# Kernel tuning notes

Measured on AMD Instinct MI355X. Metric: run time of the kernel, lower is better.

Reference implementation:

```python
import jax, jax.numpy as jnp
import numpy as np

B, N, D_MODEL, H, D_K, D_V = 4, 1024, 1024, 16, 64, 1024  # N == D_V required by the module's output matmul


def setup_inputs() -> dict:
    key = jax.random.key(0)
    ks = jax.random.split(key, 7)
    def xavier(k, shape):
        fan_in, fan_out = shape[-2], shape[-1]
        std = (2.0 / (fan_in + fan_out)) ** 0.5
        return jax.random.normal(k, shape, dtype=jnp.float32) * std
    return {
        "query": jax.random.normal(ks[0], (B, N, D_MODEL), dtype=jnp.float32),
        "key": jax.random.normal(ks[1], (B, N, D_MODEL), dtype=jnp.float32),
        "value": jax.random.normal(ks[2], (B, N, D_MODEL), dtype=jnp.float32),
        "w_q": xavier(ks[3], (H, D_MODEL, D_K)),
        "w_k": xavier(ks[4], (H, D_MODEL, D_K)),
        "w_v": xavier(ks[5], (H, D_MODEL, D_V)),
        "w_o": xavier(ks[6], (D_MODEL, H * D_V)),
    }


def reference(query, key, value, w_q, w_k, w_v, w_o):
    # Per-head projections: [B,N,d_model] x [H,d_model,d] -> [B,H,N,d]
    q = jnp.einsum('bnd,hdk->bhnk', query, w_q)
    k = jnp.einsum('bnd,hdk->bhnk', key, w_k)
    v = jnp.einsum('bnd,hdv->bhnv', value, w_v)
    scale = 1.0 / jnp.sqrt(jnp.asarray(q.shape[-1], q.dtype))
    scores = jnp.einsum('bhqk,bhmk->bhqm', q, k) * scale  # [B,H,N,N]
    weights = jax.nn.softmax(scores, axis=-1)
    out = jnp.einsum('bhqm,bhmv->bhqv', weights, v)  # [B,H,N,d_v]
    out = out.reshape(out.shape[0], -1, out.shape[-1])  # [B, H*N, d_v]
    # Faithful to source: torch.matmul(w_o, output) with w_o [d_model, H*d_v];
    # requires H*d_v == H*N (N == d_v); result [B, d_model, d_v].
    return jnp.einsum('de,bev->bdv', w_o, out)
```

## Files before the change

### kernel.cpp

```cpp
#include <hip/hip_runtime.h>
#include <hip/hip_bf16.h>

typedef __hip_bfloat16 bf16;
typedef __attribute__((ext_vector_type(8))) short short8;
typedef __attribute__((ext_vector_type(4))) float floatx4;

#define BK 64
#define LDK 72

__device__ __forceinline__ void gload_lds16(const void* g, void* l) {
    __builtin_amdgcn_global_load_lds(
        (const __attribute__((address_space(1))) void*)g,
        (__attribute__((address_space(3))) void*)l, 16, 0, 0);
}

template<bool OUT_BF16>
__global__ void __launch_bounds__(512) gemm_nt_256(
    const bf16* __restrict__ A, const bf16* __restrict__ B, void* __restrict__ Cv,
    int K, int lda, int ldb, int ldc,
    long sA, long sB, long sC)
{
    __shared__ __align__(16) bf16 As[2][256 * 64];
    __shared__ __align__(16) bf16 Bs[2][256 * 64];

    int bx = blockIdx.x, by = blockIdx.y, bz = blockIdx.z;
    if (gridDim.x == 4 && gridDim.y == 4 && (gridDim.z & 7) == 0) {
        int hw  = bx + (by << 2) + (bz << 4);
        int xcd = hw & 7;
        int idx = hw >> 3;
        int per = (int)(gridDim.z >> 3) << 4;
        int nh  = xcd * per + idx;
        bx = nh & 3; by = (nh >> 2) & 3; bz = nh >> 4;
    }

    long aoff = (long)bz * sA + (long)by * 256 * lda;
    long boff = (long)bz * sB + (long)bx * 256 * ldb;
    long coff = (long)bz * sC;

    int tid  = threadIdx.x;
    int lane = tid & 63;
    int wave = tid >> 6;
    int quad = lane >> 4;
    int l16  = lane & 15;
    int swz  = l16 & 7;
    int wm = (wave >> 2) * 128;
    int wn = (wave & 3) * 64;

    int srow   = tid >> 3;
    int schunk = (tid & 7) ^ (srow & 7);
    int dwb    = (wave << 3) * 64;

    const bf16* Asrc = A + aoff;
    const bf16* Bsrc = B + boff;

    floatx4 acc[8][4] = {};
    const int nt = K / BK;

    auto STAGE_A = [&](int db, int half, int kt) {
        long kofs = (long)kt * BK + schunk * 8;
#pragma unroll
        for (int s = 0; s < 2; s++) {
            int r = half * 128 + s * 64;
            gload_lds16(Asrc + (long)(r + srow) * lda + kofs, &As[db][r * 64 + dwb]);
        }
    };
    auto STAGE_B = [&](int db, int half, int kt) {
        long kofs = (long)kt * BK + schunk * 8;
#pragma unroll
        for (int s = 0; s < 2; s++) {
            int r = half * 128 + s * 64;
            gload_lds16(Bsrc + (long)(r + srow) * ldb + kofs, &Bs[db][r * 64 + dwb]);
        }
    };

    STAGE_A(0, 0, 0); STAGE_A(0, 1, 0); STAGE_B(0, 0, 0); STAGE_B(0, 1, 0);
    STAGE_A(1, 0, 1);
    asm volatile("s_waitcnt vmcnt(2)" ::: "memory");
    asm volatile("s_barrier" ::: "memory");

    short8 af[4][2], bf[4][2];
    int db = 0;
    for (int kt = 0; kt < nt; kt++) {
        const bf16* as = As[db];
        const bf16* bs = Bs[db];
        bool st1 = (kt + 1 < nt);
        bool st2 = (kt + 2 < nt);

#pragma unroll
        for (int i = 0; i < 4; i++)
#pragma unroll
            for (int ks = 0; ks < 2; ks++)
                af[i][ks] = *(const short8*)(&as[(wm + i * 16 + l16) * 64 + ((((ks << 2) | quad)) ^ swz) * 8]);
#pragma unroll
        for (int j = 0; j < 2; j++)
#pragma unroll
            for (int ks = 0; ks < 2; ks++)
                bf[j][ks] = *(const short8*)(&bs[(wn + j * 16 + l16) * 64 + ((((ks << 2) | quad)) ^ swz) * 8]);
        if (st1) STAGE_A(db ^ 1, 1, kt + 1);
        __builtin_amdgcn_sched_barrier(0);
        __builtin_amdgcn_s_setprio(1);
#pragma unroll
        for (int i = 0; i < 4; i++)
#pragma unroll
            for (int j = 0; j < 2; j++)
#pragma unroll
                for (int ks = 0; ks < 2; ks++)
                    acc[i][j] = __builtin_amdgcn_mfma_f32_16x16x32_bf16(af[i][ks], bf[j][ks], acc[i][j], 0, 0, 0);
        __builtin_amdgcn_s_setprio(0);
        __builtin_amdgcn_sched_barrier(0);

#pragma unroll
        for (int j = 2; j < 4; j++)
#pragma unroll
            for (int ks = 0; ks < 2; ks++)
                bf[j][ks] = *(const short8*)(&bs[(wn + j * 16 + l16) * 64 + ((((ks << 2) | quad)) ^ swz) * 8]);
        if (st1) STAGE_B(db ^ 1, 0, kt + 1);
        __builtin_amdgcn_sched_barrier(0);
        __builtin_amdgcn_s_setprio(1);
#pragma unroll
        for (int i = 0; i < 4; i++)
#pragma unroll
            for (int j = 2; j < 4; j++)
#pragma unroll
                for (int ks = 0; ks < 2; ks++)
                    acc[i][j] = __builtin_amdgcn_mfma_f32_16x16x32_bf16(af[i][ks], bf[j][ks], acc[i][j], 0, 0, 0);
        __builtin_amdgcn_s_setprio(0);
        __builtin_amdgcn_sched_barrier(0);

#pragma unroll
        for (int i = 0; i < 4; i++)
#pragma unroll
            for (int ks = 0; ks < 2; ks++)
                af[i][ks] = *(const short8*)(&as[(wm + 64 + i * 16 + l16) * 64 + ((((ks << 2) | quad)) ^ swz) * 8]);
        if (st1) STAGE_B(db ^ 1, 1, kt + 1);
        __builtin_amdgcn_sched_barrier(0);
        __builtin_amdgcn_s_setprio(1);
#pragma unroll
        for (int i = 0; i < 4; i++)
#pragma unroll
            for (int j = 2; j < 4; j++)
#pragma unroll
                for (int ks = 0; ks < 2; ks++)
                    acc[i + 4][j] = __builtin_amdgcn_mfma_f32_16x16x32_bf16(af[i][ks], bf[j][ks], acc[i + 4][j], 0, 0, 0);
        __builtin_amdgcn_s_setprio(0);
        __builtin_amdgcn_sched_barrier(0);
        asm volatile("s_barrier" ::: "memory");

        if (st2) STAGE_A(db, 0, kt + 2);
        __builtin_amdgcn_sched_barrier(0);
        __builtin_amdgcn_s_setprio(1);
#pragma unroll
        for (int i = 0; i < 4; i++)
#pragma unroll
            for (int j = 0; j < 2; j++)
#pragma unroll
                for (int ks = 0; ks < 2; ks++)
                    acc[i + 4][j] = __builtin_amdgcn_mfma_f32_16x16x32_bf16(af[i][ks], bf[j][ks], acc[i + 4][j], 0, 0, 0);
        __builtin_amdgcn_s_setprio(0);
        __builtin_amdgcn_sched_barrier(0);

        if (st2) asm volatile("s_waitcnt vmcnt(2)" ::: "memory");
        else     asm volatile("s_waitcnt vmcnt(0)" ::: "memory");
        asm volatile("s_barrier" ::: "memory");
        db ^= 1;
    }

#pragma unroll
    for (int i = 0; i < 8; i++) {
        int row = by * 256 + wm + i * 16 + quad * 4;
#pragma unroll
        for (int j = 0; j < 4; j++) {
            int col = bx * 256 + wn + j * 16 + l16;
#pragma unroll
            for (int v = 0; v < 4; v++) {
                float val = acc[i][j][v];
                if (OUT_BF16)
                    ((bf16*)Cv)[coff + (long)(row + v) * ldc + col] = __float2bfloat16(val);
                else
                    ((float*)Cv)[coff + (long)(row + v) * ldc + col] = val;
            }
        }
    }
}

template<bool OUT_BF16, bool A_F32, bool B_F32>
__global__ void __launch_bounds__(256) gemm_nt(
    const void* __restrict__ Av, const void* __restrict__ Bv, void* __restrict__ Cv,
    int M, int N, int K, int lda, int ldb, int ldc,
    long sA, long sB, long sC)
{
    __shared__ __align__(16) bf16 As[128 * LDK];
    __shared__ __align__(16) bf16 Bs[128 * LDK];

    int bx = blockIdx.x, by = blockIdx.y, bz = blockIdx.z;

    long aoff = (long)bz * sA;
    long boff = (long)bz * sB;
    long coff = (long)bz * sC;

    int m0 = by * 128;
    int n0 = bx * 128;
    int tid  = threadIdx.x;
    int lane = tid & 63;
    int wave = tid >> 6;
    int quad = lane >> 4;
    int l16  = lane & 15;
    int wm = (wave >> 1) * 64;
    int wn = (wave & 1) * 64;

    int sr = tid >> 3;
    int sc = (tid & 7) * 8;

    floatx4 acc[4][4] = {};

    uint4  pa[4], pb[4];
    float4 pa0[4], pa1[4], pb0[4], pb1[4];

    const int nt = K / BK;

#pragma unroll
    for (int s = 0; s < 4; s++) {
        int r = sr + 32 * s;
        int gm = m0 + r;
        if (A_F32) {
            const float* p = (const float*)Av + aoff + (long)gm * lda + sc;
            if (gm < M) { pa0[s] = *(const float4*)p; pa1[s] = *(const float4*)(p + 4); }
            else { pa0[s] = {0,0,0,0}; pa1[s] = {0,0,0,0}; }
        } else {
            pa[s] = (gm < M) ? *(const uint4*)((const bf16*)Av + aoff + (long)gm * lda + sc)
                             : (uint4){0,0,0,0};
        }
        int gn = n0 + r;
        if (B_F32) {
            const float* p = (const float*)Bv + boff + (long)gn * ldb + sc;
            if (gn < N) { pb0[s] = *(const float4*)p; pb1[s] = *(const float4*)(p + 4); }
            else { pb0[s] = {0,0,0,0}; pb1[s] = {0,0,0,0}; }
        } else {
            pb[s] = (gn < N) ? *(const uint4*)((const bf16*)Bv + boff + (long)gn * ldb + sc)
                             : (uint4){0,0,0,0};
        }
    }

    for (int kt = 0; kt < nt; kt++) {
        __syncthreads();
#pragma unroll
        for (int s = 0; s < 4; s++) {
            int r = sr + 32 * s;
            if (A_F32) {
                bf16 t[8];
                t[0]=__float2bfloat16(pa0[s].x); t[1]=__float2bfloat16(pa0[s].y);
                t[2]=__float2bfloat16(pa0[s].z); t[3]=__float2bfloat16(pa0[s].w);
                t[4]=__float2bfloat16(pa1[s].x); t[5]=__float2bfloat16(pa1[s].y);
                t[6]=__float2bfloat16(pa1[s].z); t[7]=__float2bfloat16(pa1[s].w);
                *(uint4*)(&As[r * LDK + sc]) = *(const uint4*)t;
            } else {
                *(uint4*)(&As[r * LDK + sc]) = pa[s];
            }
            if (B_F32) {
                bf16 t[8];
                t[0]=__float2bfloat16(pb0[s].x); t[1]=__float2bfloat16(pb0[s].y);
                t[2]=__float2bfloat16(pb0[s].z); t[3]=__float2bfloat16(pb0[s].w);
                t[4]=__float2bfloat16(pb1[s].x); t[5]=__float2bfloat16(pb1[s].y);
                t[6]=__float2bfloat16(pb1[s].z); t[7]=__float2bfloat16(pb1[s].w);
                *(uint4*)(&Bs[r * LDK + sc]) = *(const uint4*)t;
            } else {
                *(uint4*)(&Bs[r * LDK + sc]) = pb[s];
            }
        }
        __syncthreads();

        if (kt + 1 < nt) {
            int k0 = (kt + 1) * BK;
#pragma unroll
            for (int s = 0; s < 4; s++) {
                int r = sr + 32 * s;
                int gm = m0 + r;
                if (A_F32) {
                    const float* p = (const float*)Av + aoff + (long)gm * lda + k0 + sc;
                    if (gm < M) { pa0[s] = *(const float4*)p; pa1[s] = *(const float4*)(p + 4); }
                    else { pa0[s] = {0,0,0,0}; pa1[s] = {0,0,0,0}; }
                } else {
                    pa[s] = (gm < M) ? *(const uint4*)((const bf16*)Av + aoff + (long)gm * lda + k0 + sc)
                                     : (uint4){0,0,0,0};
                }
                int gn = n0 + r;
                if (B_F32) {
                    const float* p = (const float*)Bv + boff + (long)gn * ldb + k0 + sc;
                    if (gn < N) { pb0[s] = *(const float4*)p; pb1[s] = *(const float4*)(p + 4); }
                    else { pb0[s] = {0,0,0,0}; pb1[s] = {0,0,0,0}; }
                } else {
                    pb[s] = (gn < N) ? *(const uint4*)((const bf16*)Bv + boff + (long)gn * ldb + k0 + sc)
                                     : (uint4){0,0,0,0};
                }
            }
        }

#pragma unroll
        for (int ks = 0; ks < 2; ks++) {
            short8 af[4], bfr[4];
#pragma unroll
            for (int i = 0; i < 4; i++)
                af[i] = *(const short8*)(&As[(wm + i * 16 + l16) * LDK + ks * 32 + quad * 8]);
#pragma unroll
            for (int j = 0; j < 4; j++)
                bfr[j] = *(const short8*)(&Bs[(wn + j * 16 + l16) * LDK + ks * 32 + quad * 8]);
#pragma unroll
            for (int i = 0; i < 4; i++)
#pragma unroll
                for (int j = 0; j < 4; j++)
                    acc[i][j] = __builtin_amdgcn_mfma_f32_16x16x32_bf16(af[i], bfr[j], acc[i][j], 0, 0, 0);
        }
    }

#pragma unroll
    for (int i = 0; i < 4; i++) {
        int row = m0 + wm + i * 16 + quad * 4;
#pragma unroll
        for (int j = 0; j < 4; j++) {
            int col = n0 + wn + j * 16 + l16;
            if (col >= N) continue;
#pragma unroll
            for (int v = 0; v < 4; v++) {
                int r = row + v;
                if (r < M) {
                    float val = acc[i][j][v];
                    if (OUT_BF16)
                        ((bf16*)Cv)[coff + (long)r * ldc + col] = __float2bfloat16(val);
                    else
                        ((float*)Cv)[coff + (long)r * ldc + col] = val;
                }
            }
        }
    }
}

__global__ void __launch_bounds__(256) attn_softmax(
    const bf16* __restrict__ Q, const bf16* __restrict__ Kb, bf16* __restrict__ Wts)
{
    __shared__ __align__(16) bf16 Ks[64 * 72];

    int h = blockIdx.y;
    const bf16* Qbh = Q  + (long)h * 262144;
    const bf16* Kbh = Kb + (long)h * 262144;
    bf16* W = Wts + (long)h * 1048576;

    int tid  = threadIdx.x;
    int lane = tid & 63;
    int wave = tid >> 6;
    int quad = lane >> 4;
    int l16  = lane & 15;
    int q0 = blockIdx.x * 64 + wave * 16;

    short8 a0 = *(const short8*)(Qbh + (long)(q0 + l16) * 64 + quad * 8);
    short8 a1 = *(const short8*)(Qbh + (long)(q0 + l16) * 64 + 32 + quad * 8);

    int sr = tid >> 3;
    int sc = (tid & 7) * 8;

    const float scale = 0.125f;
    float m_v[4] = {-1e30f, -1e30f, -1e30f, -1e30f};
    float l_v[4] = {0.f, 0.f, 0.f, 0.f};

    for (int t = 0; t < 16; t++) {
        __syncthreads();
        const bf16* src = Kbh + (long)(t * 64 + sr) * 64 + sc;
        *(uint4*)(&Ks[sr * 72 + sc])        = *(const uint4*)src;
        *(uint4*)(&Ks[(sr + 32) * 72 + sc]) = *(const uint4*)(src + 32 * 64);
        __syncthreads();
#pragma unroll
        for (int j = 0; j < 4; j++) {
            short8 b0 = *(const short8*)(&Ks[(j * 16 + l16) * 72 + quad * 8]);
            short8 b1 = *(const short8*)(&Ks[(j * 16 + l16) * 72 + 32 + quad * 8]);
            floatx4 acc = {0.f, 0.f, 0.f, 0.f};
            acc = __builtin_amdgcn_mfma_f32_16x16x32_bf16(a0, b0, acc, 0, 0, 0);
            acc = __builtin_amdgcn_mfma_f32_16x16x32_bf16(a1, b1, acc, 0, 0, 0);
#pragma unroll
            for (int v = 0; v < 4; v++) {
                float s  = acc[v] * scale;
                float nm = fmaxf(m_v[v], s);
                l_v[v] = l_v[v] * __expf(m_v[v] - nm) + __expf(s - nm);
                m_v[v] = nm;
            }
        }
    }

#pragma unroll
    for (int d = 1; d < 16; d <<= 1) {
#pragma unroll
        for (int v = 0; v < 4; v++) {
            float om = __shfl_xor(m_v[v], d);
            float ol = __shfl_xor(l_v[v], d);
            float nm = fmaxf(m_v[v], om);
            l_v[v] = l_v[v] * __expf(m_v[v] - nm) + ol * __expf(om - nm);
            m_v[v] = nm;
        }
    }
    float linv[4];
#pragma unroll
    for (int v = 0; v < 4; v++) linv[v] = 1.0f / l_v[v];

    for (int t = 0; t < 16; t++) {
        __syncthreads();
        const bf16* src = Kbh + (long)(t * 64 + sr) * 64 + sc;
        *(uint4*)(&Ks[sr * 72 + sc])        = *(const uint4*)src;
        *(uint4*)(&Ks[(sr + 32) * 72 + sc]) = *(const uint4*)(src + 32 * 64);
        __syncthreads();
#pragma unroll
        for (int j = 0; j < 4; j++) {
            short8 b0 = *(const short8*)(&Ks[(j * 16 + l16) * 72 + quad * 8]);
            short8 b1 = *(const short8*)(&Ks[(j * 16 + l16) * 72 + 32 + quad * 8]);
            floatx4 acc = {0.f, 0.f, 0.f, 0.f};
            acc = __builtin_amdgcn_mfma_f32_16x16x32_bf16(a0, b0, acc, 0, 0, 0);
            acc = __builtin_amdgcn_mfma_f32_16x16x32_bf16(a1, b1, acc, 0, 0, 0);
#pragma unroll
            for (int v = 0; v < 4; v++) {
                float w = __expf(acc[v] * scale - m_v[v]) * linv[v];
                W[(long)(q0 + quad * 4 + v) * 1024 + t * 64 + j * 16 + l16] = __float2bfloat16(w);
            }
        }
    }
}

__global__ void __launch_bounds__(256) cast_bf16_k(
    const float* __restrict__ in, bf16* __restrict__ out, int n4)
{
    int i = blockIdx.x * 256 + threadIdx.x;
    if (i >= n4) return;
    float4 v = ((const float4*)in)[i];
    bf16 t[4] = {__float2bfloat16(v.x), __float2bfloat16(v.y),
                 __float2bfloat16(v.z), __float2bfloat16(v.w)};
    ((uint2*)out)[i] = *(const uint2*)t;
}

__global__ void __launch_bounds__(256) transpose_cast(
    const float* __restrict__ in, bf16* __restrict__ out, int R, int C)
{
    __shared__ float t[32][33];
    int h = blockIdx.z;
    const float* inh = in + (long)h * R * C;
    bf16* outh = out + (long)h * R * C;
    int c0 = blockIdx.x * 32, r0 = blockIdx.y * 32;
    int tx = threadIdx.x, ty = threadIdx.y;
#pragma unroll
    for (int i = 0; i < 32; i += 8)
        t[ty + i][tx] = inh[(long)(r0 + ty + i) * C + c0 + tx];
    __syncthreads();
#pragma unroll
    for (int i = 0; i < 32; i += 8)
        outh[(long)(c0 + ty + i) * R + r0 + tx] = __float2bfloat16(t[tx][ty + i]);
}

__global__ void __launch_bounds__(256) reduce16_k(
    const float* __restrict__ part, float* __restrict__ out)
{
    int i = blockIdx.x * 256 + threadIdx.x;
    float4 s = ((const float4*)part)[i];
#pragma unroll
    for (int c = 1; c < 16; c++) {
        float4 p = ((const float4*)part)[c * 262144 + i];
        s.x += p.x; s.y += p.y; s.z += p.z; s.w += p.w;
    }
    ((float4*)out)[i] = s;
}

extern "C" void kernel_launch(void* const* d_in, const int* in_sizes, int n_in,
                              void* d_out, int out_size, void* d_ws, size_t ws_size,
                              hipStream_t stream) {
    const float* query = (const float*)d_in[0];
    const float* key   = (const float*)d_in[1];
    const float* value = (const float*)d_in[2];
    const float* w_q   = (const float*)d_in[3];
    const float* w_k   = (const float*)d_in[4];
    const float* w_v   = (const float*)d_in[5];
    const float* w_o   = (const float*)d_in[6];
    float* out = (float*)d_out;

    char* ws = (char*)d_ws;
    const size_t MB = (size_t)1 << 20;
    bf16* wqt      = (bf16*)(ws + 0 * MB);
    bf16* wkt      = (bf16*)(ws + 2 * MB);
    bf16* wvt      = (bf16*)(ws + 4 * MB);
    bf16* wob      = (bf16*)(ws + 36 * MB);
    bf16* qb       = (bf16*)(ws + 68 * MB);
    bf16* kb       = (bf16*)(ws + 76 * MB);
    bf16* vt_b     = (bf16*)(ws + 84 * MB);
    bf16* wts_b    = (bf16*)(ws + 116 * MB);
    bf16* att_b    = (bf16*)(ws + 148 * MB);
    bf16* value_bf = (bf16*)(ws + 148 * MB);
    float* out_part = (float*)(ws + 84 * MB);

    transpose_cast<<<dim3(2, 32, 16),  dim3(32, 8), 0, stream>>>(w_q, wqt, 1024, 64);
    transpose_cast<<<dim3(2, 32, 16),  dim3(32, 8), 0, stream>>>(w_k, wkt, 1024, 64);
    transpose_cast<<<dim3(32, 32, 16), dim3(32, 8), 0, stream>>>(w_v, wvt, 1024, 1024);
    cast_bf16_k<<<16384, 256, 0, stream>>>(w_o, wob, 1024 * 16384 / 4);

    gemm_nt<true, true, false><<<dim3(1, 32, 16), 256, 0, stream>>>(
        query, wqt, qb, 4096, 64, 1024, 1024, 1024, 64, 0L, 65536L, 262144L);
    gemm_nt<true, true, false><<<dim3(1, 32, 16), 256, 0, stream>>>(
        key, wkt, kb, 4096, 64, 1024, 1024, 1024, 64, 0L, 65536L, 262144L);

    for (int b = 0; b < 4; b++) {
        cast_bf16_k<<<1024, 256, 0, stream>>>(value + (long)b * 1048576, value_bf, 262144);

        gemm_nt_256<true><<<dim3(4, 4, 16), 512, 0, stream>>>(
            wvt, value_bf, vt_b,
            1024, 1024, 1024, 1024, 1048576L, 0L, 1048576L);

        attn_softmax<<<dim3(16, 16), 256, 0, stream>>>(
            qb + (long)b * 65536, kb + (long)b * 65536, wts_b);

        gemm_nt_256<true><<<dim3(4, 4, 16), 512, 0, stream>>>(
            vt_b, wts_b, att_b,
            1024, 1024, 1024, 16384, 1048576L, 1048576L, 1024L);

        gemm_nt_256<false><<<dim3(4, 4, 16), 512, 0, stream>>>(
            wob, att_b, out_part,
            1024, 16384, 16384, 1024, 1024L, 1024L, 1048576L);

        reduce16_k<<<1024, 256, 0, stream>>>(out_part, out + (long)b * 1048576);
    }

    (void)in_sizes; (void)n_in; (void)out_size; (void)ws_size;
}
```

Measured before the change: 859.8 us.

## Deepen GEMM prefetch to two full tiles ahead with region-ordered staging

Reorganizes the global-to-LDS staging in the 256x256 bf16 GEMM so both buffers are filled up front and tile kt+2 is loaded into the current buffer as soon as each quarter of it has been consumed. Row groups of A and B are split into interleaved regions (AX/BX, then BY/AY) that match the order in which the MFMA phases read them, with waits on vmcnt(8) and barriers placed after those phases. The goal is to keep more global loads in flight and hide memory latency better. The cost is extra barriers and lgkmcnt waits inside the loop, plus tighter correctness requirements on which LDS regions are overwritten when.

```diff
diff --git a/kernel.cpp b/kernel.cpp
--- a/kernel.cpp
+++ b/kernel.cpp
@@ -48,34 +48,32 @@
 
     int srow   = tid >> 3;
     int schunk = (tid & 7) ^ (srow & 7);
-    int dwb    = (wave << 3) * 64;
 
     const bf16* Asrc = A + aoff;
     const bf16* Bsrc = B + boff;
 
+    auto STA = [&](int db, int r0, int kt) {
+        long kofs = (long)kt * BK + schunk * 8;
+        gload_lds16(Asrc + (long)(r0 + srow) * lda + kofs,
+                    &As[db][(r0 + (wave << 3)) * 64]);
+    };
+    auto STB = [&](int db, int r0, int r1, int kt) {
+        long kofs = (long)kt * BK + schunk * 8;
+        int rr = (srow < 32) ? (r0 + srow) : (r1 + srow - 32);
+        int rb = (wave < 4) ? (r0 + (wave << 3)) : (r1 + ((wave - 4) << 3));
+        gload_lds16(Bsrc + (long)rr * ldb + kofs, &Bs[db][rb * 64]);
+    };
+    auto STAGE_AX = [&](int db, int kt){ STA(db, 0, kt);  STA(db, 128, kt); };
+    auto STAGE_AY = [&](int db, int kt){ STA(db, 64, kt); STA(db, 192, kt); };
+    auto STAGE_BX = [&](int db, int kt){ STB(db, 0, 64, kt);  STB(db, 128, 192, kt); };
+    auto STAGE_BY = [&](int db, int kt){ STB(db, 32, 96, kt); STB(db, 160, 224, kt); };
+
     floatx4 acc[8][4] = {};
     const int nt = K / BK;
 
-    auto STAGE_A = [&](int db, int half, int kt) {
-        long kofs = (long)kt * BK + schunk * 8;
-#pragma unroll
-        for (int s = 0; s < 2; s++) {
-            int r = half * 128 + s * 64;
-            gload_lds16(Asrc + (long)(r + srow) * lda + kofs, &As[db][r * 64 + dwb]);
-        }
-    };
-    auto STAGE_B = [&](int db, int half, int kt) {
-        long kofs = (long)kt * BK + schunk * 8;
-#pragma unroll
-        for (int s = 0; s < 2; s++) {
-            int r = half * 128 + s * 64;
-            gload_lds16(Bsrc + (long)(r + srow) * ldb + kofs, &Bs[db][r * 64 + dwb]);
-        }
-    };
-
-    STAGE_A(0, 0, 0); STAGE_A(0, 1, 0); STAGE_B(0, 0, 0); STAGE_B(0, 1, 0);
-    STAGE_A(1, 0, 1);
-    asm volatile("s_waitcnt vmcnt(2)" ::: "memory");
+    STAGE_AX(0, 0); STAGE_BX(0, 0); STAGE_BY(0, 0); STAGE_AY(0, 0);
+    STAGE_AX(1, 1); STAGE_BX(1, 1); STAGE_BY(1, 1); STAGE_AY(1, 1);
+    asm volatile("s_waitcnt vmcnt(8)" ::: "memory");
     asm volatile("s_barrier" ::: "memory");
 
     short8 af[4][2], bf[4][2];
@@ -83,56 +81,52 @@
     for (int kt = 0; kt < nt; kt++) {
         const bf16* as = As[db];
         const bf16* bs = Bs[db];
-        bool st1 = (kt + 1 < nt);
         bool st2 = (kt + 2 < nt);
 
 #pragma unroll
         for (int i = 0; i < 4; i++)
 #pragma unroll
             for (int ks = 0; ks < 2; ks++)
-                af[i][ks] = *(const short8*)(&as[(wm + i * 16 + l16) * 64 + ((((ks << 2) | quad)) ^ swz) * 8]);
+                af[i][ks] = *(const short8*)(&as[(wm + i * 16 + l16) * 64 + (((ks << 2) | quad) ^ swz) * 8]);
 #pragma unroll
         for (int j = 0; j < 2; j++)
 #pragma unroll
             for (int ks = 0; ks < 2; ks++)
-                bf[j][ks] = *(const short8*)(&bs[(wn + j * 16 + l16) * 64 + ((((ks << 2) | quad)) ^ swz) * 8]);
-        if (st1) STAGE_A(db ^ 1, 1, kt + 1);
-        __builtin_amdgcn_sched_barrier(0);
+                bf[j][ks] = *(const short8*)(&bs[(wn + j * 16 + l16) * 64 + (((ks << 2) | quad) ^ swz) * 8]);
         __builtin_amdgcn_s_setprio(1);
 #pragma unroll
         for (int i = 0; i < 4; i++)
 #pragma unroll
             for (int j = 0; j < 2; j++)
+#pragma unroll
+                for (int ks = 0; ks < 2; ks++)
+                    acc[i][j] = __builtin_amdgcn_mfma_f32_16x16x32_bf16(af[i][ks], bf[j][ks], acc[i][j], 0, 0, 0);
+        __builtin_amdgcn_s_setprio(0);
+
+#pragma unroll
+        for (int j = 2; j < 4; j++)
+#pragma unroll
+            for (int ks = 0; ks < 2; ks++)
+                bf[j][ks] = *(const short8*)(&bs[(wn + j * 16 + l16) * 64 + (((ks << 2) | quad) ^ swz) * 8]);
+        __builtin_amdgcn_s_setprio(1);
+#pragma unroll
+        for (int i = 0; i < 4; i++)
+#pragma unroll
+            for (int j = 2; j < 4; j++)
 #pragma unroll
                 for (int ks = 0; ks < 2; ks++)
                     acc[i][j] = __builtin_amdgcn_mfma_f32_16x16x32_bf16(af[i][ks], bf[j][ks], acc[i][j], 0, 0, 0);
         __builtin_amdgcn_s_setprio(0);
         __builtin_amdgcn_sched_barrier(0);
-
-#pragma unroll
-        for (int j = 2; j < 4; j++)
+        asm volatile("s_waitcnt lgkmcnt(0)" ::: "memory");
+        asm volatile("s_barrier" ::: "memory");
+
+        if (st2) { STAGE_AX(db, kt + 2); STAGE_BX(db, kt + 2); }
+#pragma unroll
+        for (int i = 0; i < 4; i++)
 #pragma unroll
             for (int ks = 0; ks < 2; ks++)
-                bf[j][ks] = *(const short8*)(&bs[(wn + j * 16 + l16) * 64 + ((((ks << 2) | quad)) ^ swz) * 8]);
-        if (st1) STAGE_B(db ^ 1, 0, kt + 1);
-        __builtin_amdgcn_sched_barrier(0);
-        __builtin_amdgcn_s_setprio(1);
-#pragma unroll
-        for (int i = 0; i < 4; i++)
-#pragma unroll
-            for (int j = 2; j < 4; j++)
-#pragma unroll
-                for (int ks = 0; ks < 2; ks++)
-                    acc[i][j] = __builtin_amdgcn_mfma_f32_16x16x32_bf16(af[i][ks], bf[j][ks], acc[i][j], 0, 0, 0);
-        __builtin_amdgcn_s_setprio(0);
-        __builtin_amdgcn_sched_barrier(0);
-
-#pragma unroll
-        for (int i = 0; i < 4; i++)
-#pragma unroll
-            for (int ks = 0; ks < 2; ks++)
-                af[i][ks] = *(const short8*)(&as[(wm + 64 + i * 16 + l16) * 64 + ((((ks << 2) | quad)) ^ swz) * 8]);
-        if (st1) STAGE_B(db ^ 1, 1, kt + 1);
+                af[i][ks] = *(const short8*)(&as[(wm + 64 + i * 16 + l16) * 64 + (((ks << 2) | quad) ^ swz) * 8]);
         __builtin_amdgcn_sched_barrier(0);
         __builtin_amdgcn_s_setprio(1);
 #pragma unroll
@@ -144,9 +138,10 @@
                     acc[i + 4][j] = __builtin_amdgcn_mfma_f32_16x16x32_bf16(af[i][ks], bf[j][ks], acc[i + 4][j], 0, 0, 0);
         __builtin_amdgcn_s_setprio(0);
         __builtin_amdgcn_sched_barrier(0);
+        asm volatile("s_waitcnt lgkmcnt(0)" ::: "memory");
         asm volatile("s_barrier" ::: "memory");
 
-        if (st2) STAGE_A(db, 0, kt + 2);
+        if (st2) { STAGE_BY(db, kt + 2); STAGE_AY(db, kt + 2); }
         __builtin_amdgcn_sched_barrier(0);
         __builtin_amdgcn_s_setprio(1);
 #pragma unroll
@@ -159,9 +154,11 @@
         __builtin_amdgcn_s_setprio(0);
         __builtin_amdgcn_sched_barrier(0);
 
-        if (st2) asm volatile("s_waitcnt vmcnt(2)" ::: "memory");
-        else     asm volatile("s_waitcnt vmcnt(0)" ::: "memory");
-        asm volatile("s_barrier" ::: "memory");
+        if (kt + 1 < nt) {
+            if (st2) asm volatile("s_waitcnt vmcnt(8)" ::: "memory");
+            else     asm volatile("s_waitcnt vmcnt(0)" ::: "memory");
+            asm volatile("s_barrier" ::: "memory");
+        }
         db ^= 1;
     }
 
```

Measured after the change: 921.7 us. 7.2% more time.
